# Optimization experiments

Measured on AMD Instinct MI355X. Metric: run time of the kernel, lower is better.

Reference implementation:

```python
import jax, jax.numpy as jnp
import numpy as np

N = 100_000   # total nodes in batched graph
E = 800_000   # total edges
D = 64        # in_dim
H = 64        # hidden_dim
C = 10        # out_dim (num classes)
L = 3         # num_layers
G = 500       # graphs in batch
EPS = 1e-5    # BatchNorm eps


def setup_inputs() -> dict:
    key = jax.random.key(0)
    ks = jax.random.split(key, 12)
    feat = jax.random.normal(ks[0], (N, D), dtype=jnp.float32)
    src = jax.random.randint(ks[1], (E,), 0, N, dtype=jnp.int32)
    dst = jax.random.randint(ks[2], (E,), 0, N, dtype=jnp.int32)
    node2graph = jnp.sort(jax.random.randint(ks[3], (N,), 0, G, dtype=jnp.int32))
    # stacked GCN layer params (in_dim == hidden_dim so all layers share shape)
    Ws = jax.random.normal(ks[4], (L, H, H), dtype=jnp.float32) * 0.1
    bs = jax.random.normal(ks[5], (L, H), dtype=jnp.float32) * 0.01
    gammas = 1.0 + 0.1 * jax.random.normal(ks[6], (L, H), dtype=jnp.float32)
    betas = 0.1 * jax.random.normal(ks[7], (L, H), dtype=jnp.float32)
    means = 0.1 * jax.random.normal(ks[8], (L, H), dtype=jnp.float32)
    vars_ = jax.random.uniform(ks[9], (L, H), dtype=jnp.float32) + 0.5
    Wc = jax.random.normal(ks[10], (H, C), dtype=jnp.float32) * 0.1
    bc = jax.random.normal(ks[11], (C,), dtype=jnp.float32) * 0.01
    return {"feat": feat, "src": src, "dst": dst, "node2graph": node2graph,
            "Ws": Ws, "bs": bs, "gammas": gammas, "betas": betas,
            "means": means, "vars_": vars_, "Wc": Wc, "bc": bc}


def reference(feat, src, dst, node2graph, Ws, bs, gammas, betas, means, vars_, Wc, bc):
    h = feat
    for l in range(L):
        # dgl copy_src + sum: aggregate source features at destination nodes
        m = jax.ops.segment_sum(h[src], dst, num_segments=N)  # [N, H]
        h = m @ Ws[l] + bs[l]                                  # Linear
        # BatchNorm1d (eval mode, running stats)
        h = (h - means[l]) * (gammas[l] / jnp.sqrt(vars_[l] + EPS)) + betas[l]
        h = jax.nn.elu(h)
    logits = h @ Wc + bc                    # classify(h)
    logp = jax.nn.log_softmax(logits, axis=1)
    Hent = -jnp.sum(jnp.exp(logp) * logp, axis=1)   # entropy per node
    lam = 1.0 - Hent / jnp.max(Hent)                # lambda_list
    # ragged per-graph weighted sum pooling
    pooled = jax.ops.segment_sum(lam[:, None] * h, node2graph, num_segments=G)  # [G, H]
    return pooled @ Wc + bc                 # final classify (dropout eval = id)
```

## Files before the change

### kernel.cpp

```cpp
#include <hip/hip_runtime.h>
#include <hip/hip_bf16.h>
#include <math.h>

#define NNODES 100000
#define NEDGES 800000
#define HDIM 64
#define CDIM 10
#define NGRAPH 500
#define CAP 24
#define OVFCAP 16384
#define BN_EPS 1e-5f
#define TN 64

typedef __attribute__((ext_vector_type(8))) short short8;
typedef __attribute__((ext_vector_type(4))) float f32x4;

__device__ __forceinline__ float bflo(unsigned u){ return __uint_as_float(u << 16); }
__device__ __forceinline__ float bfhi(unsigned u){ return __uint_as_float(u & 0xFFFF0000u); }
__device__ __forceinline__ unsigned f2bf(float f){
    unsigned u = __float_as_uint(f);
    u += 0x7FFFu + ((u >> 16) & 1u);
    return u >> 16;
}

__global__ void cvt_feat(const float4* __restrict__ F, uint4* __restrict__ B) {
    int i = blockIdx.x * 256 + threadIdx.x;
    float4 a = F[2*i], b = F[2*i+1];
    uint4 o;
    o.x = f2bf(a.x) | (f2bf(a.y) << 16);
    o.y = f2bf(a.z) | (f2bf(a.w) << 16);
    o.z = f2bf(b.x) | (f2bf(b.y) << 16);
    o.w = f2bf(b.z) | (f2bf(b.w) << 16);
    B[i] = o;
}

__global__ void fill_buckets(const int* __restrict__ src, const int* __restrict__ dst,
                             unsigned* __restrict__ cnt, int* __restrict__ csr,
                             unsigned* __restrict__ ovfcnt, int* __restrict__ ovf) {
    int e = blockIdx.x * blockDim.x + threadIdx.x;
    if (e >= NEDGES) return;
    int d = dst[e];
    unsigned slot = atomicAdd(&cnt[d], 1u);
    if (slot < CAP) {
        csr[(size_t)d * CAP + slot] = src[e];
    } else {
        unsigned o = atomicAdd(ovfcnt, 1u);
        if (o < OVFCAP) { ovf[2*o] = src[e]; ovf[2*o+1] = d; }
    }
}

__global__ __launch_bounds__(256, 6) void layer_fused(
        const unsigned* __restrict__ hb, const unsigned* __restrict__ cnt,
        const int* __restrict__ csr, const unsigned* __restrict__ ovfcnt,
        const int* __restrict__ ovf,
        const float* __restrict__ Ws, const float* __restrict__ bs,
        const float* __restrict__ gammas, const float* __restrict__ betas,
        const float* __restrict__ means, const float* __restrict__ vars_,
        int layer, unsigned short* __restrict__ out16) {
    __shared__ unsigned short Mb[TN][72];
    __shared__ unsigned short Wt[HDIM][72];
    __shared__ float Scl[HDIM], Shl[HDIM];
    int tid = threadIdx.x;
    int base = blockIdx.x * TN;

    const float* Wg = Ws + (size_t)layer*HDIM*HDIM;
    #pragma unroll
    for (int r = 0; r < 16; ++r) {
        int f = tid + 256*r;
        int k = f >> 6, c = f & 63;
        Wt[c][k] = (unsigned short)f2bf(Wg[f]);
    }
    if (tid < HDIM) {
        int c = tid;
        float b  = bs[layer*HDIM + c];
        float gm = gammas[layer*HDIM + c];
        float be = betas[layer*HDIM + c];
        float mu = means[layer*HDIM + c];
        float vv = vars_[layer*HDIM + c];
        float s  = gm * rsqrtf(vv + BN_EPS);
        Scl[c] = s;
        Shl[c] = (b - mu) * s + be;
    }

    int grp = tid >> 3;
    int sub = tid & 7;
    const uint4* h4 = (const uint4*)hb;
    unsigned novf = *ovfcnt; if (novf > OVFCAP) novf = OVFCAP;
    #pragma unroll
    for (int i = 0; i < 2; ++i) {
        int row = grp + 32*i;
        int node = base + row;
        float a0=0,a1=0,a2=0,a3=0,a4=0,a5=0,a6=0,a7=0;
        if (node < NNODES) {
            unsigned deg = cnt[node]; if (deg > CAP) deg = CAP;
            const int* ed = csr + (size_t)node * CAP;
            unsigned e = 0;
            for (; e + 4 <= deg; e += 4) {
                int s0 = ed[e], s1 = ed[e+1], s2 = ed[e+2], s3 = ed[e+3];
                uint4 v0 = h4[(size_t)s0*8 + sub];
                uint4 v1 = h4[(size_t)s1*8 + sub];
                uint4 v2 = h4[(size_t)s2*8 + sub];
                uint4 v3 = h4[(size_t)s3*8 + sub];
                a0 += bflo(v0.x)+bflo(v1.x)+bflo(v2.x)+bflo(v3.x);
                a1 += bfhi(v0.x)+bfhi(v1.x)+bfhi(v2.x)+bfhi(v3.x);
                a2 += bflo(v0.y)+bflo(v1.y)+bflo(v2.y)+bflo(v3.y);
                a3 += bfhi(v0.y)+bfhi(v1.y)+bfhi(v2.y)+bfhi(v3.y);
                a4 += bflo(v0.z)+bflo(v1.z)+bflo(v2.z)+bflo(v3.z);
                a5 += bfhi(v0.z)+bfhi(v1.z)+bfhi(v2.z)+bfhi(v3.z);
                a6 += bflo(v0.w)+bflo(v1.w)+bflo(v2.w)+bflo(v3.w);
                a7 += bfhi(v0.w)+bfhi(v1.w)+bfhi(v2.w)+bfhi(v3.w);
            }
            for (; e < deg; ++e) {
                uint4 v = h4[(size_t)ed[e]*8 + sub];
                a0 += bflo(v.x); a1 += bfhi(v.x);
                a2 += bflo(v.y); a3 += bfhi(v.y);
                a4 += bflo(v.z); a5 += bfhi(v.z);
                a6 += bflo(v.w); a7 += bfhi(v.w);
            }
            if (novf) {
                for (unsigned o = 0; o < novf; ++o) {
                    if (ovf[2*o+1] == node) {
                        uint4 v = h4[(size_t)ovf[2*o]*8 + sub];
                        a0 += bflo(v.x); a1 += bfhi(v.x);
                        a2 += bflo(v.y); a3 += bfhi(v.y);
                        a4 += bflo(v.z); a5 += bfhi(v.z);
                        a6 += bflo(v.w); a7 += bfhi(v.w);
                    }
                }
            }
        }
        uint4 p;
        p.x = f2bf(a0) | (f2bf(a1) << 16);
        p.y = f2bf(a2) | (f2bf(a3) << 16);
        p.z = f2bf(a4) | (f2bf(a5) << 16);
        p.w = f2bf(a6) | (f2bf(a7) << 16);
        *(uint4*)&Mb[row][sub*8] = p;
    }
    __syncthreads();

    int w  = tid >> 6;
    int l  = tid & 63;
    int lr = l & 15;
    int lq = l >> 4;
    short8 a0 = *(const short8*)&Mb[w*16 + lr][lq*8];
    short8 a1 = *(const short8*)&Mb[w*16 + lr][32 + lq*8];
    f32x4 acc0 = {0.f,0.f,0.f,0.f}, acc1 = acc0, acc2 = acc0, acc3 = acc0;
    {
        short8 b0 = *(const short8*)&Wt[ 0 + lr][lq*8];
        short8 b1 = *(const short8*)&Wt[ 0 + lr][32 + lq*8];
        acc0 = __builtin_amdgcn_mfma_f32_16x16x32_bf16(a0, b0, acc0, 0, 0, 0);
        acc0 = __builtin_amdgcn_mfma_f32_16x16x32_bf16(a1, b1, acc0, 0, 0, 0);
    }
    {
        short8 b0 = *(const short8*)&Wt[16 + lr][lq*8];
        short8 b1 = *(const short8*)&Wt[16 + lr][32 + lq*8];
        acc1 = __builtin_amdgcn_mfma_f32_16x16x32_bf16(a0, b0, acc1, 0, 0, 0);
        acc1 = __builtin_amdgcn_mfma_f32_16x16x32_bf16(a1, b1, acc1, 0, 0, 0);
    }
    {
        short8 b0 = *(const short8*)&Wt[32 + lr][lq*8];
        short8 b1 = *(const short8*)&Wt[32 + lr][32 + lq*8];
        acc2 = __builtin_amdgcn_mfma_f32_16x16x32_bf16(a0, b0, acc2, 0, 0, 0);
        acc2 = __builtin_amdgcn_mfma_f32_16x16x32_bf16(a1, b1, acc2, 0, 0, 0);
    }
    {
        short8 b0 = *(const short8*)&Wt[48 + lr][lq*8];
        short8 b1 = *(const short8*)&Wt[48 + lr][32 + lq*8];
        acc3 = __builtin_amdgcn_mfma_f32_16x16x32_bf16(a0, b0, acc3, 0, 0, 0);
        acc3 = __builtin_amdgcn_mfma_f32_16x16x32_bf16(a1, b1, acc3, 0, 0, 0);
    }

    #pragma unroll
    for (int t = 0; t < 4; ++t) {
        f32x4 a = (t==0)?acc0:(t==1)?acc1:(t==2)?acc2:acc3;
        int col = t*16 + lr;
        float s = Scl[col], sh = Shl[col];
        #pragma unroll
        for (int r = 0; r < 4; ++r) {
            int node = base + w*16 + lq*4 + r;
            if (node < NNODES) {
                float y = a[r]*s + sh;
                y = (y > 0.f) ? y : expm1f(y);
                out16[(size_t)node*HDIM + col] = (unsigned short)f2bf(y);
            }
        }
    }
}

__global__ __launch_bounds__(256) void classify_bf16(
        const uint4* __restrict__ h4, const float* __restrict__ Wc,
        const float* __restrict__ bc, float* __restrict__ Hent,
        unsigned* __restrict__ maxH) {
    __shared__ float Wl[HDIM*11];
    __shared__ float bl[CDIM];
    __shared__ float wmax[4];
    int tid = threadIdx.x;
    for (int idx = tid; idx < HDIM*CDIM; idx += 256)
        Wl[(idx/CDIM)*11 + (idx%CDIM)] = Wc[idx];
    if (tid < CDIM) bl[tid] = bc[tid];
    __syncthreads();

    int node = blockIdx.x * 32 + (tid >> 3);
    int sub  = tid & 7;
    uint4 v = h4[(size_t)node*8 + sub];
    float h[8];
    h[0]=bflo(v.x); h[1]=bfhi(v.x); h[2]=bflo(v.y); h[3]=bfhi(v.y);
    h[4]=bflo(v.z); h[5]=bfhi(v.z); h[6]=bflo(v.w); h[7]=bfhi(v.w);

    float lg[CDIM];
    #pragma unroll
    for (int c = 0; c < CDIM; ++c) lg[c] = 0.f;
    #pragma unroll
    for (int k = 0; k < 8; ++k) {
        const float* wr = &Wl[(sub*8 + k)*11];
        float x = h[k];
        #pragma unroll
        for (int c = 0; c < CDIM; ++c) lg[c] += x * wr[c];
    }
    #pragma unroll
    for (int m = 1; m < 8; m <<= 1)
        #pragma unroll
        for (int c = 0; c < CDIM; ++c) lg[c] += __shfl_xor(lg[c], m, 64);
    #pragma unroll
    for (int c = 0; c < CDIM; ++c) lg[c] += bl[c];

    float mx = lg[0];
    #pragma unroll
    for (int c = 1; c < CDIM; ++c) mx = fmaxf(mx, lg[c]);
    float se = 0.f, dot = 0.f;
    #pragma unroll
    for (int c = 0; c < CDIM; ++c) { float e = expf(lg[c]-mx); se += e; dot += e*lg[c]; }
    float Hv = (mx + logf(se)) - dot/se;
    Hv = fmaxf(Hv, 0.f);
    if (sub == 0) Hent[node] = Hv;

    float m8 = Hv;
    #pragma unroll
    for (int m = 8; m < 64; m <<= 1) m8 = fmaxf(m8, __shfl_xor(m8, m, 64));
    if ((tid & 63) == 0) wmax[tid >> 6] = m8;
    __syncthreads();
    if (tid == 0) {
        float mm = fmaxf(fmaxf(wmax[0], wmax[1]), fmaxf(wmax[2], wmax[3]));
        atomicMax(maxH, __float_as_uint(mm));
    }
}

__global__ void pool_final_bf16(const unsigned* __restrict__ H2, const float* __restrict__ Hent,
                                const unsigned* __restrict__ maxH, const int* __restrict__ n2g,
                                const float* __restrict__ Wc, const float* __restrict__ bc,
                                float* __restrict__ out) {
    __shared__ float partial[8][HDIM];
    __shared__ float pooled[HDIM];
    int g = blockIdx.x;
    int tid = threadIdx.x;

    int lo = 0, hi = NNODES;
    while (lo < hi) { int mid = (lo+hi) >> 1; if (n2g[mid] < g) lo = mid+1; else hi = mid; }
    int start = lo;
    hi = NNODES;
    while (lo < hi) { int mid = (lo+hi) >> 1; if (n2g[mid] < g+1) lo = mid+1; else hi = mid; }
    int end = lo;

    float invMax = 1.0f / __uint_as_float(*maxH);
    int half = tid >> 5, l = tid & 31;
    float ax = 0.f, ay = 0.f;
    for (int i = start + half; i < end; i += 8) {
        float lam = 1.0f - Hent[i] * invMax;
        unsigned u = H2[(size_t)i*32 + l];
        ax += lam * bflo(u);
        ay += lam * bfhi(u);
    }
    partial[half][2*l]   = ax;
    partial[half][2*l+1] = ay;
    __syncthreads();
    if (tid < HDIM) {
        float s = 0.f;
        #pragma unroll
        for (int hh = 0; hh < 8; ++hh) s += partial[hh][tid];
        pooled[tid] = s;
    }
    __syncthreads();
    if (tid < CDIM) {
        float s = bc[tid];
        for (int k = 0; k < HDIM; ++k) s += pooled[k] * Wc[k*CDIM + tid];
        out[g*CDIM + tid] = s;
    }
}

extern "C" void kernel_launch(void* const* d_in, const int* in_sizes, int n_in,
                              void* d_out, int out_size, void* d_ws, size_t ws_size,
                              hipStream_t stream) {
    const float* feat  = (const float*)d_in[0];
    const int*   src   = (const int*)d_in[1];
    const int*   dst   = (const int*)d_in[2];
    const int*   n2g   = (const int*)d_in[3];
    const float* Ws    = (const float*)d_in[4];
    const float* bs    = (const float*)d_in[5];
    const float* gam   = (const float*)d_in[6];
    const float* bet   = (const float*)d_in[7];
    const float* mea   = (const float*)d_in[8];
    const float* var_  = (const float*)d_in[9];
    const float* Wc    = (const float*)d_in[10];
    const float* bc    = (const float*)d_in[11];
    float* out = (float*)d_out;

    char* ws = (char*)d_ws;
    size_t off = 0;
    auto take = [&](size_t bytes) {
        char* p = ws + off;
        off += (bytes + 255) & ~(size_t)255;
        return p;
    };

    unsigned* cnt    = (unsigned*)take((size_t)NNODES*4);
    unsigned* ovfcnt = (unsigned*)take(4);
    unsigned* maxH   = (unsigned*)take(4);
    int*      ovf    = (int*)take((size_t)OVFCAP*2*4);
    float*    Hent   = (float*)take((size_t)NNODES*4);
    unsigned* featb  = (unsigned*)take((size_t)NNODES*HDIM*2);
    unsigned* HA     = (unsigned*)take((size_t)NNODES*HDIM*2);
    unsigned* HB     = (unsigned*)take((size_t)NNODES*HDIM*2);
    int*      csr    = (int*)take((size_t)NNODES*CAP*4);

    hipMemsetAsync(cnt, 0, (size_t)NNODES*4, stream);
    hipMemsetAsync(ovfcnt, 0, 4, stream);
    hipMemsetAsync(maxH, 0, 4, stream);

    cvt_feat<<<(NNODES*HDIM/8 + 255)/256, 256, 0, stream>>>((const float4*)feat, (uint4*)featb);
    fill_buckets<<<(NEDGES+255)/256, 256, 0, stream>>>(src, dst, cnt, csr, ovfcnt, ovf);

    int grid = (NNODES + TN - 1) / TN;
    layer_fused<<<grid, 256, 0, stream>>>(featb, cnt, csr, ovfcnt, ovf,
                                          Ws, bs, gam, bet, mea, var_, 0, (unsigned short*)HA);
    layer_fused<<<grid, 256, 0, stream>>>((const unsigned*)HA, cnt, csr, ovfcnt, ovf,
                                          Ws, bs, gam, bet, mea, var_, 1, (unsigned short*)HB);
    layer_fused<<<grid, 256, 0, stream>>>((const unsigned*)HB, cnt, csr, ovfcnt, ovf,
                                          Ws, bs, gam, bet, mea, var_, 2, (unsigned short*)HA);

    classify_bf16<<<(NNODES+31)/32, 256, 0, stream>>>((const uint4*)HA, Wc, bc, Hent, maxH);
    pool_final_bf16<<<NGRAPH, 256, 0, stream>>>(HA, Hent, maxH, n2g, Wc, bc, out);
}
```

Measured before the change: 196.2 us.

## Fuse feature conversion with edge bucketing, shrink bucket cap, templatize layer kernel

Merges the bf16 feature conversion and the edge bucket fill into one launch, relying on N*D/8 equaling E so each thread does one of each. Reduces the per-node bucket capacity from 24 to 16, which shrinks the CSR footprint but sends more edges to the overflow list that every node scans linearly. Also templatizes the layer kernel on layer index, raises launch-bounds occupancy, vectorizes the neighbor index load as int4, and uses atomicExch for CSR stores. The smaller cap risks heavy overflow scans, since Poisson(8) degrees above 16 are not rare across 100k nodes.

Result: slower. 590.3 us (+200.9%).

```diff
diff --git a/kernel.cpp b/kernel.cpp
--- a/kernel.cpp
+++ b/kernel.cpp
@@ -7,7 +7,7 @@
 #define HDIM 64
 #define CDIM 10
 #define NGRAPH 500
-#define CAP 24
+#define CAP 16
 #define OVFCAP 16384
 #define BN_EPS 1e-5f
 #define TN 64
@@ -23,7 +23,10 @@
     return u >> 16;
 }
 
-__global__ void cvt_feat(const float4* __restrict__ F, uint4* __restrict__ B) {
+__global__ void prep_fill(const float4* __restrict__ F, uint4* __restrict__ B,
+                          const int* __restrict__ src, const int* __restrict__ dst,
+                          unsigned* __restrict__ cnt, int* __restrict__ csr,
+                          unsigned* __restrict__ ovfcnt, int* __restrict__ ovf) {
     int i = blockIdx.x * 256 + threadIdx.x;
     float4 a = F[2*i], b = F[2*i+1];
     uint4 o;
@@ -32,38 +35,32 @@
     o.z = f2bf(b.x) | (f2bf(b.y) << 16);
     o.w = f2bf(b.z) | (f2bf(b.w) << 16);
     B[i] = o;
-}
-
-__global__ void fill_buckets(const int* __restrict__ src, const int* __restrict__ dst,
-                             unsigned* __restrict__ cnt, int* __restrict__ csr,
-                             unsigned* __restrict__ ovfcnt, int* __restrict__ ovf) {
-    int e = blockIdx.x * blockDim.x + threadIdx.x;
-    if (e >= NEDGES) return;
-    int d = dst[e];
+    int d = dst[i], s = src[i];
     unsigned slot = atomicAdd(&cnt[d], 1u);
     if (slot < CAP) {
-        csr[(size_t)d * CAP + slot] = src[e];
+        atomicExch(&csr[(size_t)d * CAP + slot], s);
     } else {
-        unsigned o = atomicAdd(ovfcnt, 1u);
-        if (o < OVFCAP) { ovf[2*o] = src[e]; ovf[2*o+1] = d; }
-    }
-}
-
-__global__ __launch_bounds__(256, 6) void layer_fused(
+        unsigned oo = atomicAdd(ovfcnt, 1u);
+        if (oo < OVFCAP) { ovf[2*oo] = s; ovf[2*oo+1] = d; }
+    }
+}
+
+template<int LAYER>
+__global__ __launch_bounds__(256, 8) void layer_fused(
         const unsigned* __restrict__ hb, const unsigned* __restrict__ cnt,
         const int* __restrict__ csr, const unsigned* __restrict__ ovfcnt,
         const int* __restrict__ ovf,
         const float* __restrict__ Ws, const float* __restrict__ bs,
         const float* __restrict__ gammas, const float* __restrict__ betas,
         const float* __restrict__ means, const float* __restrict__ vars_,
-        int layer, unsigned short* __restrict__ out16) {
+        unsigned short* __restrict__ out16) {
     __shared__ unsigned short Mb[TN][72];
     __shared__ unsigned short Wt[HDIM][72];
     __shared__ float Scl[HDIM], Shl[HDIM];
     int tid = threadIdx.x;
     int base = blockIdx.x * TN;
 
-    const float* Wg = Ws + (size_t)layer*HDIM*HDIM;
+    const float* Wg = Ws + (size_t)LAYER*HDIM*HDIM;
     #pragma unroll
     for (int r = 0; r < 16; ++r) {
         int f = tid + 256*r;
@@ -72,11 +69,11 @@
     }
     if (tid < HDIM) {
         int c = tid;
-        float b  = bs[layer*HDIM + c];
-        float gm = gammas[layer*HDIM + c];
-        float be = betas[layer*HDIM + c];
-        float mu = means[layer*HDIM + c];
-        float vv = vars_[layer*HDIM + c];
+        float b  = bs[LAYER*HDIM + c];
+        float gm = gammas[LAYER*HDIM + c];
+        float be = betas[LAYER*HDIM + c];
+        float mu = means[LAYER*HDIM + c];
+        float vv = vars_[LAYER*HDIM + c];
         float s  = gm * rsqrtf(vv + BN_EPS);
         Scl[c] = s;
         Shl[c] = (b - mu) * s + be;
@@ -96,11 +93,11 @@
             const int* ed = csr + (size_t)node * CAP;
             unsigned e = 0;
             for (; e + 4 <= deg; e += 4) {
-                int s0 = ed[e], s1 = ed[e+1], s2 = ed[e+2], s3 = ed[e+3];
-                uint4 v0 = h4[(size_t)s0*8 + sub];
-                uint4 v1 = h4[(size_t)s1*8 + sub];
-                uint4 v2 = h4[(size_t)s2*8 + sub];
-                uint4 v3 = h4[(size_t)s3*8 + sub];
+                int4 iv = *(const int4*)(ed + e);
+                uint4 v0 = h4[(size_t)iv.x*8 + sub];
+                uint4 v1 = h4[(size_t)iv.y*8 + sub];
+                uint4 v2 = h4[(size_t)iv.z*8 + sub];
+                uint4 v3 = h4[(size_t)iv.w*8 + sub];
                 a0 += bflo(v0.x)+bflo(v1.x)+bflo(v2.x)+bflo(v3.x);
                 a1 += bfhi(v0.x)+bfhi(v1.x)+bfhi(v2.x)+bfhi(v3.x);
                 a2 += bflo(v0.y)+bflo(v1.y)+bflo(v2.y)+bflo(v3.y);
@@ -129,12 +126,12 @@
                 }
             }
         }
-        uint4 p;
-        p.x = f2bf(a0) | (f2bf(a1) << 16);
-        p.y = f2bf(a2) | (f2bf(a3) << 16);
-        p.z = f2bf(a4) | (f2bf(a5) << 16);
-        p.w = f2bf(a6) | (f2bf(a7) << 16);
-        *(uint4*)&Mb[row][sub*8] = p;
+        uint4 pk;
+        pk.x = f2bf(a0) | (f2bf(a1) << 16);
+        pk.y = f2bf(a2) | (f2bf(a3) << 16);
+        pk.z = f2bf(a4) | (f2bf(a5) << 16);
+        pk.w = f2bf(a6) | (f2bf(a7) << 16);
+        *(uint4*)&Mb[row][sub*8] = pk;
     }
     __syncthreads();
 
@@ -326,16 +323,16 @@
     hipMemsetAsync(ovfcnt, 0, 4, stream);
     hipMemsetAsync(maxH, 0, 4, stream);
 
-    cvt_feat<<<(NNODES*HDIM/8 + 255)/256, 256, 0, stream>>>((const float4*)feat, (uint4*)featb);
-    fill_buckets<<<(NEDGES+255)/256, 256, 0, stream>>>(src, dst, cnt, csr, ovfcnt, ovf);
+    prep_fill<<<NEDGES/256, 256, 0, stream>>>((const float4*)feat, (uint4*)featb,
+                                              src, dst, cnt, csr, ovfcnt, ovf);
 
     int grid = (NNODES + TN - 1) / TN;
-    layer_fused<<<grid, 256, 0, stream>>>(featb, cnt, csr, ovfcnt, ovf,
-                                          Ws, bs, gam, bet, mea, var_, 0, (unsigned short*)HA);
-    layer_fused<<<grid, 256, 0, stream>>>((const unsigned*)HA, cnt, csr, ovfcnt, ovf,
-                                          Ws, bs, gam, bet, mea, var_, 1, (unsigned short*)HB);
-    layer_fused<<<grid, 256, 0, stream>>>((const unsigned*)HB, cnt, csr, ovfcnt, ovf,
-                                          Ws, bs, gam, bet, mea, var_, 2, (unsigned short*)HA);
+    layer_fused<0><<<grid, 256, 0, stream>>>(featb, cnt, csr, ovfcnt, ovf,
+                                             Ws, bs, gam, bet, mea, var_, (unsigned short*)HA);
+    layer_fused<1><<<grid, 256, 0, stream>>>((const unsigned*)HA, cnt, csr, ovfcnt, ovf,
+                                             Ws, bs, gam, bet, mea, var_, (unsigned short*)HB);
+    layer_fused<2><<<grid, 256, 0, stream>>>((const unsigned*)HB, cnt, csr, ovfcnt, ovf,
+                                             Ws, bs, gam, bet, mea, var_, (unsigned short*)HA);
 
     classify_bf16<<<(NNODES+31)/32, 256, 0, stream>>>((const uint4*)HA, Wc, bc, Hent, maxH);
     pool_final_bf16<<<NGRAPH, 256, 0, stream>>>(HA, Hent, maxH, n2g, Wc, bc, out);
```
